# Kernel optimization log

Hardware: AMD Instinct MI355X
Metric: run time of the kernel (lower is better)

Reference implementation:

```python
import jax, jax.numpy as jnp
import numpy as np

NUM_MAX_PATHS = 10
LANE_FEAT_DIM = 128
SEQ_LEN = 80
BATCH = 256

def setup_inputs() -> dict:
    key = jax.random.key(0)
    ks = jax.random.split(key, 8)
    H = LANE_FEAT_DIM
    return {
        "agent_past_motion_context": jax.random.normal(ks[0], (BATCH, 128), dtype=jnp.float32),
        "possible_lanes": jax.random.normal(ks[1], (SEQ_LEN, BATCH * NUM_MAX_PATHS, 2), dtype=jnp.float32),
        "W_emb": jax.random.normal(ks[2], (H, 5), dtype=jnp.float32) * 0.1,
        "b_emb": jax.random.normal(ks[3], (H,), dtype=jnp.float32) * 0.1,
        "W_ih": jax.random.normal(ks[4], (4 * H, H), dtype=jnp.float32) * 0.1,
        "W_hh": jax.random.normal(ks[5], (4 * H, H), dtype=jnp.float32) * 0.1,
        "b_ih": jax.random.normal(ks[6], (4 * H,), dtype=jnp.float32) * 0.1,
        "b_hh": jax.random.normal(ks[7], (4 * H,), dtype=jnp.float32) * 0.1,
    }

def _lane_features(lanes):
    # lanes: [S, BL, 2]. Build 5-dim feature: (x, y, dx, dy, yaw).
    diff = lanes[1:] - lanes[:-1]                        # [S-1, BL, 2]
    diff = jnp.concatenate([jnp.zeros_like(lanes[:1]), diff], axis=0)
    # yaw = atan2(y, x) vs reference vector (1, 0)
    yaw = jnp.arctan2(lanes[..., 1], lanes[..., 0])      # [S, BL]
    ext = jnp.concatenate([lanes, diff, yaw[..., None]], axis=-1)  # [S, BL, 5]
    # lanes containing any NaN produce all-zero features (original conditional)
    valid = jnp.logical_not(jnp.any(jnp.isnan(lanes), axis=(0, 2)))  # [BL]
    return jnp.where(valid[None, :, None], ext, 0.0)

def _lstm(emb, W_ih, W_hh, b_ih, b_hh):
    H = W_hh.shape[1]
    BL = emb.shape[1]
    # precompute input projections for all steps: [S, BL, 4H]
    x_proj = jnp.einsum('sbi,gi->sbg', emb, W_ih) + b_ih

    def step(carry, xg):
        h, c = carry
        gates = xg + h @ W_hh.T + b_hh
        i, f, g, o = jnp.split(gates, 4, axis=-1)
        c = jax.nn.sigmoid(f) * c + jax.nn.sigmoid(i) * jnp.tanh(g)
        h = jax.nn.sigmoid(o) * jnp.tanh(c)
        return (h, c), None

    h0 = jnp.zeros((BL, H), dtype=emb.dtype)
    (h, c), _ = jax.lax.scan(step, (h0, h0), x_proj)
    return h

def reference(agent_past_motion_context, possible_lanes, W_emb, b_emb, W_ih, W_hh, b_ih, b_hh):
    b = agent_past_motion_context.shape[0]
    BL = possible_lanes.shape[1]
    num_max_paths = BL // b
    H = W_emb.shape[0]
    ext = _lane_features(possible_lanes)                         # [S, BL, 5]
    emb = jax.nn.relu(ext @ W_emb.T + b_emb)                     # [S, BL, H]
    h = _lstm(emb, W_ih, W_hh, b_ih, b_hh)                       # [BL, H]
    return h.reshape(b, num_max_paths, H)
```

## Files before the change

### kernel.cpp

```cpp
#include <hip/hip_runtime.h>
#include <stdint.h>

#define S_LEN 80
#define H_DIM 128
#define ROWS 10
#define MROWS 16
#define BLOCK_T 512

typedef __bf16 bf16x8 __attribute__((ext_vector_type(8)));
typedef unsigned short u16x8 __attribute__((ext_vector_type(8)));
typedef unsigned short u16x4 __attribute__((ext_vector_type(4)));
typedef float f32x4 __attribute__((ext_vector_type(4)));

__device__ __forceinline__ unsigned short f2bf(float f) {
    uint32_t u = __builtin_bit_cast(uint32_t, f);
    u += 0x7FFFu + ((u >> 16) & 1u);
    return (unsigned short)(u >> 16);
}
__device__ __forceinline__ float sigf(float x) {
    return __builtin_amdgcn_rcpf(1.0f + __expf(-x));
}
__device__ __forceinline__ float thf(float x) {
    return 2.0f * __builtin_amdgcn_rcpf(1.0f + __expf(-2.0f * x)) - 1.0f;
}

__global__ __launch_bounds__(BLOCK_T, 2)
void lane_lstm(const float* __restrict__ lanes,
               const float* __restrict__ W_emb, const float* __restrict__ b_emb,
               const float* __restrict__ W_ih,  const float* __restrict__ W_hh,
               const float* __restrict__ b_ih,  const float* __restrict__ b_hh,
               float* __restrict__ out, int BL)
{
    __shared__ __align__(16) float ext_lds[S_LEN * ROWS * 5];
    __shared__ __align__(16) unsigned short emb_lds[2][MROWS * H_DIM];
    __shared__ __align__(16) unsigned short h_lds[2][MROWS * H_DIM];
    __shared__ int valid_lds[MROWS];

    const int t    = threadIdx.x;
    const int lane = t & 63;
    const int wv   = t >> 6;
    const int row0 = blockIdx.x * ROWS;

    if (t < MROWS) valid_lds[t] = 1;
    {
        u16x4 z = {0, 0, 0, 0};
        *(u16x4*)((char*)&h_lds[0][0] + t * 8) = z;
    }
    __syncthreads();

    for (int p = t; p < S_LEN * ROWS; p += BLOCK_T) {
        int s = p / ROWS;
        int r = p - s * ROWS;
        int bl = row0 + r;
        float x = 0.f, y = 0.f, dx = 0.f, dy = 0.f;
        if (bl < BL) {
            const float* lp = lanes + ((size_t)s * BL + bl) * 2;
            x = lp[0]; y = lp[1];
            if (s > 0) {
                const float* lq = lanes + ((size_t)(s - 1) * BL + bl) * 2;
                dx = x - lq[0]; dy = y - lq[1];
            }
            if (__builtin_isnan(x) || __builtin_isnan(y)) valid_lds[r] = 0;
        }
        float* e = &ext_lds[p * 5];
        e[0] = x; e[1] = y; e[2] = dx; e[3] = dy; e[4] = atan2f(y, x);
    }

    const int hcol = wv * 16 + (lane & 15);
    const int kb0  = (lane >> 4) << 3;
    f32x4 wih[4][4], whh[4][4];
    float bia[4];
    #pragma unroll
    for (int g = 0; g < 4; ++g) {
        bia[g] = b_ih[g * H_DIM + hcol] + b_hh[g * H_DIM + hcol];
        #pragma unroll
        for (int kt = 0; kt < 4; ++kt) {
            const float* pa = &W_ih[(size_t)(g * H_DIM + hcol) * H_DIM + kt * 32 + kb0];
            const float* pb = &W_hh[(size_t)(g * H_DIM + hcol) * H_DIM + kt * 32 + kb0];
            u16x8 ta, tb;
            #pragma unroll
            for (int j = 0; j < 8; ++j) { ta[j] = f2bf(pa[j]); tb[j] = f2bf(pb[j]); }
            wih[g][kt] = __builtin_bit_cast(f32x4, ta);
            whh[g][kt] = __builtin_bit_cast(f32x4, tb);
        }
    }
    #pragma unroll
    for (int g = 0; g < 4; ++g) {
        #pragma unroll
        for (int kt = 0; kt < 4; ++kt) {
            asm volatile("" : "+a"(wih[g][kt]));
            asm volatile("" : "+a"(whh[g][kt]));
        }
    }

    const int er  = t >> 5;
    const int ec0 = (t & 31) << 2;
    float wemb[4][5], bemb[4];
    #pragma unroll
    for (int j = 0; j < 4; ++j) {
        #pragma unroll
        for (int d = 0; d < 5; ++d) wemb[j][d] = W_emb[(ec0 + j) * 5 + d];
        bemb[j] = b_emb[ec0 + j];
    }
    const int ebyte = ((er << 8) + (ec0 << 1)) ^ ((er & 7) << 4);

    auto emb_store = [&](int s, int b) {
        float x0 = 0.f, x1 = 0.f, x2 = 0.f, x3 = 0.f, x4 = 0.f;
        if (er < ROWS && valid_lds[er] && row0 + er < BL) {
            const float* e = &ext_lds[(s * ROWS + er) * 5];
            x0 = e[0]; x1 = e[1]; x2 = e[2]; x3 = e[3]; x4 = e[4];
        }
        u16x4 ev;
        #pragma unroll
        for (int j = 0; j < 4; ++j) {
            float a = bemb[j];
            a += wemb[j][0] * x0; a += wemb[j][1] * x1; a += wemb[j][2] * x2;
            a += wemb[j][3] * x3; a += wemb[j][4] * x4;
            ev[j] = f2bf(fmaxf(a, 0.f));
        }
        *(u16x4*)((char*)&emb_lds[b][0] + ebyte) = ev;
    };

    __syncthreads();
    emb_store(0, 0);
    __syncthreads();

    const int arow  = lane & 15;
    const int akey  = (arow & 7) << 4;
    const int abase = (arow << 8) + ((lane >> 4) << 4);
    const int crow  = (lane >> 4) << 2;

    float c0 = 0.f, c1 = 0.f, c2 = 0.f, c3 = 0.f;

    for (int s = 0; s < S_LEN; ++s) {
        const char* eb = (const char*)&emb_lds[s & 1][0];
        const char* hb = (const char*)&h_lds[s & 1][0];

        f32x4 a0 = {bia[0], bia[0], bia[0], bia[0]};
        f32x4 a1 = {bia[1], bia[1], bia[1], bia[1]};
        f32x4 a2 = {bia[2], bia[2], bia[2], bia[2]};
        f32x4 a3 = {bia[3], bia[3], bia[3], bia[3]};

        #pragma unroll
        for (int kt = 0; kt < 4; ++kt) {
            const int aoff = (abase + kt * 64) ^ akey;
            bf16x8 ae = *(const bf16x8*)(eb + aoff);
            bf16x8 ah = *(const bf16x8*)(hb + aoff);
            a0 = __builtin_amdgcn_mfma_f32_16x16x32_bf16(ae, __builtin_bit_cast(bf16x8, wih[0][kt]), a0, 0, 0, 0);
            a0 = __builtin_amdgcn_mfma_f32_16x16x32_bf16(ah, __builtin_bit_cast(bf16x8, whh[0][kt]), a0, 0, 0, 0);
            a1 = __builtin_amdgcn_mfma_f32_16x16x32_bf16(ae, __builtin_bit_cast(bf16x8, wih[1][kt]), a1, 0, 0, 0);
            a1 = __builtin_amdgcn_mfma_f32_16x16x32_bf16(ah, __builtin_bit_cast(bf16x8, whh[1][kt]), a1, 0, 0, 0);
            a2 = __builtin_amdgcn_mfma_f32_16x16x32_bf16(ae, __builtin_bit_cast(bf16x8, wih[2][kt]), a2, 0, 0, 0);
            a2 = __builtin_amdgcn_mfma_f32_16x16x32_bf16(ah, __builtin_bit_cast(bf16x8, whh[2][kt]), a2, 0, 0, 0);
            a3 = __builtin_amdgcn_mfma_f32_16x16x32_bf16(ae, __builtin_bit_cast(bf16x8, wih[3][kt]), a3, 0, 0, 0);
            a3 = __builtin_amdgcn_mfma_f32_16x16x32_bf16(ah, __builtin_bit_cast(bf16x8, whh[3][kt]), a3, 0, 0, 0);
        }

        if (s + 1 < S_LEN) emb_store(s + 1, (s + 1) & 1);

        char* hn = (char*)&h_lds[(s + 1) & 1][0];
        float hv0, hv1, hv2, hv3;
        c0 = sigf(a1[0]) * c0 + sigf(a0[0]) * thf(a2[0]);  hv0 = sigf(a3[0]) * thf(c0);
        c1 = sigf(a1[1]) * c1 + sigf(a0[1]) * thf(a2[1]);  hv1 = sigf(a3[1]) * thf(c1);
        c2 = sigf(a1[2]) * c2 + sigf(a0[2]) * thf(a2[2]);  hv2 = sigf(a3[2]) * thf(c2);
        c3 = sigf(a1[3]) * c3 + sigf(a0[3]) * thf(a2[3]);  hv3 = sigf(a3[3]) * thf(c3);

        #pragma unroll
        for (int i = 0; i < 4; ++i) {
            const float hvi = (i == 0) ? hv0 : (i == 1) ? hv1 : (i == 2) ? hv2 : hv3;
            const int r = crow + i;
            const int byte = ((r << 8) + (hcol << 1)) ^ ((r & 7) << 4);
            *(unsigned short*)(hn + byte) = f2bf(hvi);
        }

        if (s == S_LEN - 1) {
            #pragma unroll
            for (int i = 0; i < 4; ++i) {
                const float hvi = (i == 0) ? hv0 : (i == 1) ? hv1 : (i == 2) ? hv2 : hv3;
                const int r = crow + i;
                if (r < ROWS && row0 + r < BL)
                    out[(size_t)(row0 + r) * H_DIM + hcol] = hvi;
            }
        }
        __syncthreads();
    }
}

extern "C" void kernel_launch(void* const* d_in, const int* in_sizes, int n_in,
                              void* d_out, int out_size, void* d_ws, size_t ws_size,
                              hipStream_t stream) {
    const float* lanes = (const float*)d_in[1];
    const float* W_emb = (const float*)d_in[2];
    const float* b_emb = (const float*)d_in[3];
    const float* W_ih  = (const float*)d_in[4];
    const float* W_hh  = (const float*)d_in[5];
    const float* b_ih  = (const float*)d_in[6];
    const float* b_hh  = (const float*)d_in[7];
    float* out = (float*)d_out;

    const int BL   = in_sizes[1] / (2 * S_LEN);
    const int grid = (BL + ROWS - 1) / ROWS;

    lane_lstm<<<dim3(grid), dim3(BLOCK_T), 0, stream>>>(
        lanes, W_emb, b_emb, W_ih, W_hh, b_ih, b_hh, out, BL);
}
```

Before: 128.7 us.

## Software-pipeline input projection one step ahead and fold log2e scaling into weights

Computes the input-side MFMA projection for step s+1 during step s, so only the 16 recurrent-weight MFMAs sit on the serial critical path before the activations. The -log2(e) and -2·log2(e) factors are folded into the bf16 weights and biases, so sigmoid and tanh can use the raw exp2 instruction without an extra multiply. It also switches to the native bf16 conversion and issues MFMAs through inline asm that reads the weights directly from AGPRs. The embedding store now runs two steps ahead, and the weights pick up extra rounding error from being pre-scaled before bf16 conversion.

```diff
diff --git a/kernel.cpp b/kernel.cpp
--- a/kernel.cpp
+++ b/kernel.cpp
@@ -7,22 +7,26 @@
 #define MROWS 16
 #define BLOCK_T 512
 
+#define NL2E  (-1.44269504088896f)
+#define N2L2E (-2.88539008177793f)
+
 typedef __bf16 bf16x8 __attribute__((ext_vector_type(8)));
 typedef unsigned short u16x8 __attribute__((ext_vector_type(8)));
 typedef unsigned short u16x4 __attribute__((ext_vector_type(4)));
 typedef float f32x4 __attribute__((ext_vector_type(4)));
 
-__device__ __forceinline__ unsigned short f2bf(float f) {
-    uint32_t u = __builtin_bit_cast(uint32_t, f);
-    u += 0x7FFFu + ((u >> 16) & 1u);
-    return (unsigned short)(u >> 16);
-}
-__device__ __forceinline__ float sigf(float x) {
-    return __builtin_amdgcn_rcpf(1.0f + __expf(-x));
-}
-__device__ __forceinline__ float thf(float x) {
-    return 2.0f * __builtin_amdgcn_rcpf(1.0f + __expf(-2.0f * x)) - 1.0f;
-}
+__device__ __forceinline__ float sigy(float y) {
+    return __builtin_amdgcn_rcpf(1.0f + __builtin_amdgcn_exp2f(y));
+}
+__device__ __forceinline__ float tanhy(float y) {
+    return 2.0f * __builtin_amdgcn_rcpf(1.0f + __builtin_amdgcn_exp2f(y)) - 1.0f;
+}
+__device__ __forceinline__ unsigned short bfbits(float f) {
+    return __builtin_bit_cast(unsigned short, (__bf16)f);
+}
+
+#define MFMA16(acc, va, wb) \
+    asm("v_mfma_f32_16x16x32_bf16 %0, %1, %2, %0" : "+v"(acc) : "v"(va), "a"(wb))
 
 __global__ __launch_bounds__(BLOCK_T, 2)
 void lane_lstm(const float* __restrict__ lanes,
@@ -72,14 +76,15 @@
     float bia[4];
     #pragma unroll
     for (int g = 0; g < 4; ++g) {
-        bia[g] = b_ih[g * H_DIM + hcol] + b_hh[g * H_DIM + hcol];
+        const float sc = (g == 2) ? N2L2E : NL2E;
+        bia[g] = (b_ih[g * H_DIM + hcol] + b_hh[g * H_DIM + hcol]) * sc;
         #pragma unroll
         for (int kt = 0; kt < 4; ++kt) {
             const float* pa = &W_ih[(size_t)(g * H_DIM + hcol) * H_DIM + kt * 32 + kb0];
             const float* pb = &W_hh[(size_t)(g * H_DIM + hcol) * H_DIM + kt * 32 + kb0];
             u16x8 ta, tb;
             #pragma unroll
-            for (int j = 0; j < 8; ++j) { ta[j] = f2bf(pa[j]); tb[j] = f2bf(pb[j]); }
+            for (int j = 0; j < 8; ++j) { ta[j] = bfbits(pa[j] * sc); tb[j] = bfbits(pb[j] * sc); }
             wih[g][kt] = __builtin_bit_cast(f32x4, ta);
             whh[g][kt] = __builtin_bit_cast(f32x4, tb);
         }
@@ -116,61 +121,91 @@
             float a = bemb[j];
             a += wemb[j][0] * x0; a += wemb[j][1] * x1; a += wemb[j][2] * x2;
             a += wemb[j][3] * x3; a += wemb[j][4] * x4;
-            ev[j] = f2bf(fmaxf(a, 0.f));
+            ev[j] = bfbits(fmaxf(a, 0.f));
         }
         *(u16x4*)((char*)&emb_lds[b][0] + ebyte) = ev;
     };
-
-    __syncthreads();
-    emb_store(0, 0);
-    __syncthreads();
 
     const int arow  = lane & 15;
     const int akey  = (arow & 7) << 4;
     const int abase = (arow << 8) + ((lane >> 4) << 4);
     const int crow  = (lane >> 4) << 2;
 
+    __syncthreads();
+    emb_store(0, 0);
+    __syncthreads();
+
+    f32x4 xp0 = {bia[0], bia[0], bia[0], bia[0]};
+    f32x4 xp1 = {bia[1], bia[1], bia[1], bia[1]};
+    f32x4 xp2 = {bia[2], bia[2], bia[2], bia[2]};
+    f32x4 xp3 = {bia[3], bia[3], bia[3], bia[3]};
+    {
+        const char* eb = (const char*)&emb_lds[0][0];
+        #pragma unroll
+        for (int kt = 0; kt < 4; ++kt) {
+            bf16x8 ae = *(const bf16x8*)(eb + ((abase + kt * 64) ^ akey));
+            MFMA16(xp0, ae, wih[0][kt]);
+            MFMA16(xp1, ae, wih[1][kt]);
+            MFMA16(xp2, ae, wih[2][kt]);
+            MFMA16(xp3, ae, wih[3][kt]);
+        }
+    }
+    emb_store(1, 1);
+    __syncthreads();
+
     float c0 = 0.f, c1 = 0.f, c2 = 0.f, c3 = 0.f;
 
     for (int s = 0; s < S_LEN; ++s) {
-        const char* eb = (const char*)&emb_lds[s & 1][0];
         const char* hb = (const char*)&h_lds[s & 1][0];
-
-        f32x4 a0 = {bia[0], bia[0], bia[0], bia[0]};
-        f32x4 a1 = {bia[1], bia[1], bia[1], bia[1]};
-        f32x4 a2 = {bia[2], bia[2], bia[2], bia[2]};
-        f32x4 a3 = {bia[3], bia[3], bia[3], bia[3]};
-
-        #pragma unroll
-        for (int kt = 0; kt < 4; ++kt) {
-            const int aoff = (abase + kt * 64) ^ akey;
-            bf16x8 ae = *(const bf16x8*)(eb + aoff);
-            bf16x8 ah = *(const bf16x8*)(hb + aoff);
-            a0 = __builtin_amdgcn_mfma_f32_16x16x32_bf16(ae, __builtin_bit_cast(bf16x8, wih[0][kt]), a0, 0, 0, 0);
-            a0 = __builtin_amdgcn_mfma_f32_16x16x32_bf16(ah, __builtin_bit_cast(bf16x8, whh[0][kt]), a0, 0, 0, 0);
-            a1 = __builtin_amdgcn_mfma_f32_16x16x32_bf16(ae, __builtin_bit_cast(bf16x8, wih[1][kt]), a1, 0, 0, 0);
-            a1 = __builtin_amdgcn_mfma_f32_16x16x32_bf16(ah, __builtin_bit_cast(bf16x8, whh[1][kt]), a1, 0, 0, 0);
-            a2 = __builtin_amdgcn_mfma_f32_16x16x32_bf16(ae, __builtin_bit_cast(bf16x8, wih[2][kt]), a2, 0, 0, 0);
-            a2 = __builtin_amdgcn_mfma_f32_16x16x32_bf16(ah, __builtin_bit_cast(bf16x8, whh[2][kt]), a2, 0, 0, 0);
-            a3 = __builtin_amdgcn_mfma_f32_16x16x32_bf16(ae, __builtin_bit_cast(bf16x8, wih[3][kt]), a3, 0, 0, 0);
-            a3 = __builtin_amdgcn_mfma_f32_16x16x32_bf16(ah, __builtin_bit_cast(bf16x8, whh[3][kt]), a3, 0, 0, 0);
-        }
-
-        if (s + 1 < S_LEN) emb_store(s + 1, (s + 1) & 1);
+        const char* en = (const char*)&emb_lds[(s + 1) & 1][0];
+
+        bf16x8 ah0 = *(const bf16x8*)(hb + ((abase + 0 * 64) ^ akey));
+        bf16x8 ah1 = *(const bf16x8*)(hb + ((abase + 1 * 64) ^ akey));
+        bf16x8 ah2 = *(const bf16x8*)(hb + ((abase + 2 * 64) ^ akey));
+        bf16x8 ah3 = *(const bf16x8*)(hb + ((abase + 3 * 64) ^ akey));
+        f32x4 g0 = xp0, g1 = xp1, g2 = xp2, g3 = xp3;
+        MFMA16(g0, ah0, whh[0][0]); MFMA16(g1, ah0, whh[1][0]);
+        MFMA16(g2, ah0, whh[2][0]); MFMA16(g3, ah0, whh[3][0]);
+        MFMA16(g0, ah1, whh[0][1]); MFMA16(g1, ah1, whh[1][1]);
+        MFMA16(g2, ah1, whh[2][1]); MFMA16(g3, ah1, whh[3][1]);
+        MFMA16(g0, ah2, whh[0][2]); MFMA16(g1, ah2, whh[1][2]);
+        MFMA16(g2, ah2, whh[2][2]); MFMA16(g3, ah2, whh[3][2]);
+        MFMA16(g0, ah3, whh[0][3]); MFMA16(g1, ah3, whh[1][3]);
+        MFMA16(g2, ah3, whh[2][3]); MFMA16(g3, ah3, whh[3][3]);
+
+        if (s + 1 < S_LEN) {
+            bf16x8 ae0 = *(const bf16x8*)(en + ((abase + 0 * 64) ^ akey));
+            bf16x8 ae1 = *(const bf16x8*)(en + ((abase + 1 * 64) ^ akey));
+            bf16x8 ae2 = *(const bf16x8*)(en + ((abase + 2 * 64) ^ akey));
+            bf16x8 ae3 = *(const bf16x8*)(en + ((abase + 3 * 64) ^ akey));
+            xp0 = (f32x4){bia[0], bia[0], bia[0], bia[0]};
+            xp1 = (f32x4){bia[1], bia[1], bia[1], bia[1]};
+            xp2 = (f32x4){bia[2], bia[2], bia[2], bia[2]};
+            xp3 = (f32x4){bia[3], bia[3], bia[3], bia[3]};
+            MFMA16(xp0, ae0, wih[0][0]); MFMA16(xp1, ae0, wih[1][0]);
+            MFMA16(xp2, ae0, wih[2][0]); MFMA16(xp3, ae0, wih[3][0]);
+            MFMA16(xp0, ae1, wih[0][1]); MFMA16(xp1, ae1, wih[1][1]);
+            MFMA16(xp2, ae1, wih[2][1]); MFMA16(xp3, ae1, wih[3][1]);
+            MFMA16(xp0, ae2, wih[0][2]); MFMA16(xp1, ae2, wih[1][2]);
+            MFMA16(xp2, ae2, wih[2][2]); MFMA16(xp3, ae2, wih[3][2]);
+            MFMA16(xp0, ae3, wih[0][3]); MFMA16(xp1, ae3, wih[1][3]);
+            MFMA16(xp2, ae3, wih[2][3]); MFMA16(xp3, ae3, wih[3][3]);
+            if (s + 2 < S_LEN) emb_store(s + 2, s & 1);
+        }
 
         char* hn = (char*)&h_lds[(s + 1) & 1][0];
         float hv0, hv1, hv2, hv3;
-        c0 = sigf(a1[0]) * c0 + sigf(a0[0]) * thf(a2[0]);  hv0 = sigf(a3[0]) * thf(c0);
-        c1 = sigf(a1[1]) * c1 + sigf(a0[1]) * thf(a2[1]);  hv1 = sigf(a3[1]) * thf(c1);
-        c2 = sigf(a1[2]) * c2 + sigf(a0[2]) * thf(a2[2]);  hv2 = sigf(a3[2]) * thf(c2);
-        c3 = sigf(a1[3]) * c3 + sigf(a0[3]) * thf(a2[3]);  hv3 = sigf(a3[3]) * thf(c3);
+        c0 = sigy(g1[0]) * c0 + sigy(g0[0]) * tanhy(g2[0]);  hv0 = sigy(g3[0]) * tanhy(c0 * N2L2E);
+        c1 = sigy(g1[1]) * c1 + sigy(g0[1]) * tanhy(g2[1]);  hv1 = sigy(g3[1]) * tanhy(c1 * N2L2E);
+        c2 = sigy(g1[2]) * c2 + sigy(g0[2]) * tanhy(g2[2]);  hv2 = sigy(g3[2]) * tanhy(c2 * N2L2E);
+        c3 = sigy(g1[3]) * c3 + sigy(g0[3]) * tanhy(g2[3]);  hv3 = sigy(g3[3]) * tanhy(c3 * N2L2E);
 
         #pragma unroll
         for (int i = 0; i < 4; ++i) {
             const float hvi = (i == 0) ? hv0 : (i == 1) ? hv1 : (i == 2) ? hv2 : hv3;
             const int r = crow + i;
             const int byte = ((r << 8) + (hcol << 1)) ^ ((r & 7) << 4);
-            *(unsigned short*)(hn + byte) = f2bf(hvi);
+            *(unsigned short*)(hn + byte) = bfbits(hvi);
         }
 
         if (s == S_LEN - 1) {
```

After: 116.7 us. 9.4% less time.
